# Performance work log

Hardware: AMD Instinct MI355X
Metric: run time of the kernel (lower is better)

## Reference

```python
import jax, jax.numpy as jnp
import numpy as np

EPS = 1e-6
SIGMA_C = 2.0
PAD = 0
VOCAB = 100
D_EMB = 384


def setup_inputs() -> dict:
    key = jax.random.key(0)
    k1, k2, k3 = jax.random.split(key, 3)
    B, L = 32, 1025  # L odd so durs[:,1::2] and durs[:,2::2] align
    text = jax.random.randint(k1, (B, L), 0, VOCAB)
    durs = jax.random.randint(k2, (B, L), 0, 4)
    emb_table = jax.random.normal(k3, (VOCAB, D_EMB), dtype=jnp.float32)
    return {"text": text, "durs": durs, "emb_table": emb_table, "total_time": 2048}


def reference(text, durs, emb_table, total_time):
    # --- merge blank/token pairs (as in GaussianEmbedding.forward) ---
    text_m = jnp.concatenate([text[:, :1], text[:, 1::2]], axis=1)              # [B,N]
    durs_m = jnp.concatenate([durs[:, :1], durs[:, 1::2] + durs[:, 2::2]], axis=1)  # [B,N]
    embed = emb_table[text_m]                                                    # [B,N,E]

    # --- Gaussian length regulation ---
    d = durs_m.astype(jnp.float32)
    cum = jnp.cumsum(d, axis=-1)                 # [B,N] end times
    c = cum - 0.5 * d                            # [B,N] token centers
    sig = d / SIGMA_C + EPS                      # [B,N]
    t = jnp.arange(total_time, dtype=jnp.float32) + 0.5  # [T] frame midpoints

    # Normal pdf weights [B,T,N]
    z = (t[None, :, None] - c[:, None, :]) / sig[:, None, :]
    w = jnp.exp(-0.5 * z * z) / (sig[:, None, :] * jnp.sqrt(2.0 * jnp.pi))
    # zero weight for pad tokens, normalize over tokens
    w = jnp.where((text_m == PAD)[:, None, :], 0.0, w)
    w = w / (w.sum(-1, keepdims=True) + EPS)
    # zero frames beyond each sample's total duration
    valid = t[None, :] < cum[:, -1:]             # [B,T]
    w = jnp.where(valid[..., None], w, 0.0)

    return jnp.einsum('btn,bne->bte', w, embed)  # [B,T,E]
```

## Files before the change

### kernel.cpp

```cpp
#include <hip/hip_runtime.h>
#include <hip/hip_bf16.h>

#define BATCH 32
#define LSEQ 1025
#define TT 2048
#define NTOK 513
#define EMB 384
#define FT 32
#define WMAX 64
#define INV_SQRT_2PI 0.3989422804014327f

__device__ inline float* scan513(float* src, float* dst) {
  for (int off = 1; off < NTOK; off <<= 1) {
    for (int i = threadIdx.x; i < NTOK; i += 256) {
      float v = src[i];
      if (i >= off) v += src[i - off];
      dst[i] = v;
    }
    __syncthreads();
    float* t = src; src = dst; dst = t;
  }
  return src;
}

__global__ __launch_bounds__(256) void prep_kernel(
    const int* __restrict__ text, const int* __restrict__ durs,
    float2* __restrict__ kept, int* __restrict__ counts,
    float* __restrict__ totals) {
  const int b = blockIdx.x;
  const int tid = threadIdx.x;
  __shared__ float s_a[NTOK], s_b[NTOK];
  __shared__ float s_c[NTOK];
  __shared__ float s_d[NTOK];
  __shared__ int s_tok[NTOK];

  const int* tb = text + b * LSEQ;
  const int* db = durs + b * LSEQ;
  for (int n = tid; n < NTOK; n += 256) {
    int dm, tk;
    if (n == 0) { dm = db[0]; tk = tb[0]; }
    else { dm = db[2 * n - 1] + db[2 * n]; tk = tb[2 * n - 1]; }
    s_d[n] = (float)dm;
    s_a[n] = (float)dm;
    s_tok[n] = tk;
  }
  __syncthreads();
  float* cum = scan513(s_a, s_b);
  for (int n = tid; n < NTOK; n += 256) {
    s_c[n] = cum[n] - 0.5f * s_d[n];
  }
  if (tid == 0) totals[b] = cum[NTOK - 1];
  __syncthreads();
  float* flagbuf = (cum == s_a) ? s_a : s_b;
  float* other = (cum == s_a) ? s_b : s_a;
  for (int n = tid; n < NTOK; n += 256) {
    flagbuf[n] = (s_d[n] >= 1.0f && s_tok[n] != 0) ? 1.0f : 0.0f;
  }
  __syncthreads();
  float* incl = scan513(flagbuf, other);
  for (int n = tid; n < NTOK; n += 256) {
    float d = s_d[n];
    int tk = s_tok[n];
    if (d >= 1.0f && tk != 0) {
      int pos = (int)incl[n] - 1;
      int packed = ((int)d << 17) | (tk * EMB);
      kept[b * NTOK + pos] = make_float2(s_c[n], __int_as_float(packed));
    }
  }
  if (tid == 0) counts[b] = (int)incl[NTOK - 1];
}

__global__ __launch_bounds__(384) void frames_kernel(
    const float2* __restrict__ kept, const int* __restrict__ counts,
    const float* __restrict__ totals, const float* __restrict__ emb,
    float* __restrict__ out) {
  const int t0 = blockIdx.x * FT;
  const int b = blockIdx.y;
  const int tid = threadIdx.x;
  const int g = tid / 96;
  const int q = tid % 96;
  const int fbase = g * 8;

  __shared__ float4 s_tk[WMAX];
  __shared__ float s_w[WMAX][FT];
  __shared__ float s_sum[FT];
  __shared__ int s_cnt;

  const int M = counts[b];
  const float total = totals[b];
  const float2* kb = kept + b * NTOK;

  const float tileLo = (float)t0 + 0.5f;
  const float tileHi = (float)t0 + 31.5f;
  const bool tile_valid = tileLo < total;

  int lo = 0, hi = 0;
  if (tile_valid) {
    const float loB = (float)t0 - 40.5f;
    const float hiB = (float)t0 + 72.5f;
    int l = 0, r = M;
    while (l < r) { int m = (l + r) >> 1; if (kb[m].x < loB) l = m + 1; else r = m; }
    lo = l;
    r = M;
    while (l < r) { int m = (l + r) >> 1; if (kb[m].x <= hiB) l = m + 1; else r = m; }
    hi = l;
  }

  if (tid < FT) s_sum[tid] = 0.f;

  float4 acc[8];
#pragma unroll
  for (int k = 0; k < 8; ++k) acc[k] = make_float4(0.f, 0.f, 0.f, 0.f);

  const float t0f = (float)t0 + 0.5f;

  for (int pos = lo; pos < hi; pos += WMAX) {
    const int cand = min(hi - pos, WMAX);
    __syncthreads();
    if (tid < 64) {
      bool touch = false;
      float cc = 0.f, df = 0.f;
      int packed = 0;
      if (tid < cand) {
        float2 kv = kb[pos + tid];
        cc = kv.x;
        packed = __float_as_int(kv.y);
        df = (float)(packed >> 17);
        const float reach = 6.7f * df + 1e-4f;
        touch = (cc + reach >= tileLo) && (cc - reach <= tileHi);
      }
      const unsigned long long mask = __ballot(touch);
      if (touch) {
        const int slot = __popcll(mask & ((1ull << (tid & 63)) - 1));
        const float inv_sig = 1.0f / (0.5f * df + 1e-6f);
        s_tk[slot] = make_float4(cc, inv_sig, INV_SQRT_2PI * inv_sig,
                                 __int_as_float(packed & 0x1FFFF));
      }
      if (tid == 0) s_cnt = __popcll(mask);
    }
    __syncthreads();
    const int cnt = s_cnt;

    const int pairs = cnt * FT;
    for (int idx = tid; idx < pairs; idx += 384) {
      const int n = idx >> 5, f = idx & (FT - 1);
      const float4 tk = s_tk[n];
      const float z = (t0f + (float)f - tk.x) * tk.y;
      s_w[n][f] = tk.z * __expf(-0.5f * z * z);
    }
    __syncthreads();

    if (tid < FT) {
      float s = 0.f;
      for (int n = 0; n < cnt; ++n) s += s_w[n][tid];
      s_sum[tid] += s;
    }

    for (int n = 0; n < cnt; ++n) {
      const float4 tk = s_tk[n];
      const float4 v = *(const float4*)(emb + __float_as_int(tk.w) + q * 4);
      const float4 w0 = *(const float4*)&s_w[n][fbase];
      const float4 w1 = *(const float4*)&s_w[n][fbase + 4];
      acc[0].x += w0.x * v.x; acc[0].y += w0.x * v.y;
      acc[0].z += w0.x * v.z; acc[0].w += w0.x * v.w;
      acc[1].x += w0.y * v.x; acc[1].y += w0.y * v.y;
      acc[1].z += w0.y * v.z; acc[1].w += w0.y * v.w;
      acc[2].x += w0.z * v.x; acc[2].y += w0.z * v.y;
      acc[2].z += w0.z * v.z; acc[2].w += w0.z * v.w;
      acc[3].x += w0.w * v.x; acc[3].y += w0.w * v.y;
      acc[3].z += w0.w * v.z; acc[3].w += w0.w * v.w;
      acc[4].x += w1.x * v.x; acc[4].y += w1.x * v.y;
      acc[4].z += w1.x * v.z; acc[4].w += w1.x * v.w;
      acc[5].x += w1.y * v.x; acc[5].y += w1.y * v.y;
      acc[5].z += w1.y * v.z; acc[5].w += w1.y * v.w;
      acc[6].x += w1.z * v.x; acc[6].y += w1.z * v.y;
      acc[6].z += w1.z * v.z; acc[6].w += w1.z * v.w;
      acc[7].x += w1.w * v.x; acc[7].y += w1.w * v.y;
      acc[7].z += w1.w * v.z; acc[7].w += w1.w * v.w;
    }
  }
  __syncthreads();

  float* obase = out + ((size_t)b * TT + t0 + fbase) * EMB + q * 4;
#pragma unroll
  for (int k = 0; k < 8; ++k) {
    const float tf = t0f + (float)(fbase + k);
    const float fac = (tf < total) ? 1.0f / (s_sum[fbase + k] + 1e-6f) : 0.0f;
    *(float4*)(obase + (size_t)k * EMB) =
        make_float4(acc[k].x * fac, acc[k].y * fac,
                    acc[k].z * fac, acc[k].w * fac);
  }
}

extern "C" void kernel_launch(void* const* d_in, const int* in_sizes, int n_in,
                              void* d_out, int out_size, void* d_ws,
                              size_t ws_size, hipStream_t stream) {
  const int* text = (const int*)d_in[0];
  const int* durs = (const int*)d_in[1];
  const float* emb = (const float*)d_in[2];
  float* out = (float*)d_out;

  float2* kept = (float2*)d_ws;
  int* counts = (int*)(kept + BATCH * NTOK);
  float* totals = (float*)(counts + BATCH);

  prep_kernel<<<BATCH, 256, 0, stream>>>(text, durs, kept, counts, totals);
  frames_kernel<<<dim3(TT / FT, BATCH), 384, 0, stream>>>(kept, counts, totals,
                                                          emb, out);
}
```

Measured before the change: 139.1 us.

## Halve frame tile, load token window once, fold weight sums into registers

Frame tiles shrink from 32 to 16 frames per block, with 192 threads per block and twice as many blocks. The per-chunk ballot/compaction loop is replaced by a single load of the whole candidate token window, capped at 104 entries. The per-frame normalisation sum is now accumulated in registers by each thread rather than in a shared-memory reduction. This removes several barriers and the serial sum pass, but any window wider than 104 tokens is silently truncated, and tokens outside the reach test now cost extra exp and FMA work.

```diff
diff --git a/kernel.cpp b/kernel.cpp
--- a/kernel.cpp
+++ b/kernel.cpp
@@ -6,8 +6,8 @@
 #define TT 2048
 #define NTOK 513
 #define EMB 384
-#define FT 32
-#define WMAX 64
+#define FT 16
+#define WMAX 104
 #define INV_SQRT_2PI 0.3989422804014327f
 
 __device__ inline float* scan513(float* src, float* dst) {
@@ -70,7 +70,7 @@
   if (tid == 0) counts[b] = (int)incl[NTOK - 1];
 }
 
-__global__ __launch_bounds__(384) void frames_kernel(
+__global__ __launch_bounds__(192) void frames_kernel(
     const float2* __restrict__ kept, const int* __restrict__ counts,
     const float* __restrict__ totals, const float* __restrict__ emb,
     float* __restrict__ out) {
@@ -83,109 +83,83 @@
 
   __shared__ float4 s_tk[WMAX];
   __shared__ float s_w[WMAX][FT];
-  __shared__ float s_sum[FT];
-  __shared__ int s_cnt;
 
   const int M = counts[b];
   const float total = totals[b];
   const float2* kb = kept + b * NTOK;
+  const float t0f = (float)t0 + 0.5f;
 
-  const float tileLo = (float)t0 + 0.5f;
-  const float tileHi = (float)t0 + 31.5f;
-  const bool tile_valid = tileLo < total;
-
-  int lo = 0, hi = 0;
-  if (tile_valid) {
+  int lo = 0, win = 0;
+  if (t0f < total) {
     const float loB = (float)t0 - 40.5f;
-    const float hiB = (float)t0 + 72.5f;
+    const float hiB = (float)t0 + 56.5f;
     int l = 0, r = M;
     while (l < r) { int m = (l + r) >> 1; if (kb[m].x < loB) l = m + 1; else r = m; }
     lo = l;
     r = M;
     while (l < r) { int m = (l + r) >> 1; if (kb[m].x <= hiB) l = m + 1; else r = m; }
-    hi = l;
+    win = l - lo;
+    if (win > WMAX) win = WMAX;
   }
 
-  if (tid < FT) s_sum[tid] = 0.f;
+  if (tid < win) {
+    float2 kv = kb[lo + tid];
+    int packed = __float_as_int(kv.y);
+    float df = (float)(packed >> 17);
+    float inv_sig = 1.0f / (0.5f * df + 1e-6f);
+    s_tk[tid] = make_float4(kv.x, inv_sig, INV_SQRT_2PI * inv_sig,
+                            __int_as_float(packed & 0x1FFFF));
+  }
+  __syncthreads();
+
+  const int pairs = win * FT;
+  for (int idx = tid; idx < pairs; idx += 192) {
+    const int n = idx >> 4, f = idx & (FT - 1);
+    const float4 tk = s_tk[n];
+    const float z = (t0f + (float)f - tk.x) * tk.y;
+    s_w[n][f] = tk.z * __expf(-0.5f * z * z);
+  }
+  __syncthreads();
 
   float4 acc[8];
+  float wsum[8];
 #pragma unroll
-  for (int k = 0; k < 8; ++k) acc[k] = make_float4(0.f, 0.f, 0.f, 0.f);
+  for (int k = 0; k < 8; ++k) {
+    acc[k] = make_float4(0.f, 0.f, 0.f, 0.f);
+    wsum[k] = 0.f;
+  }
 
-  const float t0f = (float)t0 + 0.5f;
-
-  for (int pos = lo; pos < hi; pos += WMAX) {
-    const int cand = min(hi - pos, WMAX);
-    __syncthreads();
-    if (tid < 64) {
-      bool touch = false;
-      float cc = 0.f, df = 0.f;
-      int packed = 0;
-      if (tid < cand) {
-        float2 kv = kb[pos + tid];
-        cc = kv.x;
-        packed = __float_as_int(kv.y);
-        df = (float)(packed >> 17);
-        const float reach = 6.7f * df + 1e-4f;
-        touch = (cc + reach >= tileLo) && (cc - reach <= tileHi);
-      }
-      const unsigned long long mask = __ballot(touch);
-      if (touch) {
-        const int slot = __popcll(mask & ((1ull << (tid & 63)) - 1));
-        const float inv_sig = 1.0f / (0.5f * df + 1e-6f);
-        s_tk[slot] = make_float4(cc, inv_sig, INV_SQRT_2PI * inv_sig,
-                                 __int_as_float(packed & 0x1FFFF));
-      }
-      if (tid == 0) s_cnt = __popcll(mask);
-    }
-    __syncthreads();
-    const int cnt = s_cnt;
-
-    const int pairs = cnt * FT;
-    for (int idx = tid; idx < pairs; idx += 384) {
-      const int n = idx >> 5, f = idx & (FT - 1);
-      const float4 tk = s_tk[n];
-      const float z = (t0f + (float)f - tk.x) * tk.y;
-      s_w[n][f] = tk.z * __expf(-0.5f * z * z);
-    }
-    __syncthreads();
-
-    if (tid < FT) {
-      float s = 0.f;
-      for (int n = 0; n < cnt; ++n) s += s_w[n][tid];
-      s_sum[tid] += s;
-    }
-
-    for (int n = 0; n < cnt; ++n) {
-      const float4 tk = s_tk[n];
-      const float4 v = *(const float4*)(emb + __float_as_int(tk.w) + q * 4);
-      const float4 w0 = *(const float4*)&s_w[n][fbase];
-      const float4 w1 = *(const float4*)&s_w[n][fbase + 4];
-      acc[0].x += w0.x * v.x; acc[0].y += w0.x * v.y;
-      acc[0].z += w0.x * v.z; acc[0].w += w0.x * v.w;
-      acc[1].x += w0.y * v.x; acc[1].y += w0.y * v.y;
-      acc[1].z += w0.y * v.z; acc[1].w += w0.y * v.w;
-      acc[2].x += w0.z * v.x; acc[2].y += w0.z * v.y;
-      acc[2].z += w0.z * v.z; acc[2].w += w0.z * v.w;
-      acc[3].x += w0.w * v.x; acc[3].y += w0.w * v.y;
-      acc[3].z += w0.w * v.z; acc[3].w += w0.w * v.w;
-      acc[4].x += w1.x * v.x; acc[4].y += w1.x * v.y;
-      acc[4].z += w1.x * v.z; acc[4].w += w1.x * v.w;
-      acc[5].x += w1.y * v.x; acc[5].y += w1.y * v.y;
-      acc[5].z += w1.y * v.z; acc[5].w += w1.y * v.w;
-      acc[6].x += w1.z * v.x; acc[6].y += w1.z * v.y;
-      acc[6].z += w1.z * v.z; acc[6].w += w1.z * v.w;
-      acc[7].x += w1.w * v.x; acc[7].y += w1.w * v.y;
-      acc[7].z += w1.w * v.z; acc[7].w += w1.w * v.w;
-    }
+#pragma unroll 2
+  for (int n = 0; n < win; ++n) {
+    const float4 tk = s_tk[n];
+    const float4 v = *(const float4*)(emb + __float_as_int(tk.w) + q * 4);
+    const float4 w0 = *(const float4*)&s_w[n][fbase];
+    const float4 w1 = *(const float4*)&s_w[n][fbase + 4];
+    wsum[0] += w0.x; wsum[1] += w0.y; wsum[2] += w0.z; wsum[3] += w0.w;
+    wsum[4] += w1.x; wsum[5] += w1.y; wsum[6] += w1.z; wsum[7] += w1.w;
+    acc[0].x += w0.x * v.x; acc[0].y += w0.x * v.y;
+    acc[0].z += w0.x * v.z; acc[0].w += w0.x * v.w;
+    acc[1].x += w0.y * v.x; acc[1].y += w0.y * v.y;
+    acc[1].z += w0.y * v.z; acc[1].w += w0.y * v.w;
+    acc[2].x += w0.z * v.x; acc[2].y += w0.z * v.y;
+    acc[2].z += w0.z * v.z; acc[2].w += w0.z * v.w;
+    acc[3].x += w0.w * v.x; acc[3].y += w0.w * v.y;
+    acc[3].z += w0.w * v.z; acc[3].w += w0.w * v.w;
+    acc[4].x += w1.x * v.x; acc[4].y += w1.x * v.y;
+    acc[4].z += w1.x * v.z; acc[4].w += w1.x * v.w;
+    acc[5].x += w1.y * v.x; acc[5].y += w1.y * v.y;
+    acc[5].z += w1.y * v.z; acc[5].w += w1.y * v.w;
+    acc[6].x += w1.z * v.x; acc[6].y += w1.z * v.y;
+    acc[6].z += w1.z * v.z; acc[6].w += w1.z * v.w;
+    acc[7].x += w1.w * v.x; acc[7].y += w1.w * v.y;
+    acc[7].z += w1.w * v.z; acc[7].w += w1.w * v.w;
   }
-  __syncthreads();
 
   float* obase = out + ((size_t)b * TT + t0 + fbase) * EMB + q * 4;
 #pragma unroll
   for (int k = 0; k < 8; ++k) {
     const float tf = t0f + (float)(fbase + k);
-    const float fac = (tf < total) ? 1.0f / (s_sum[fbase + k] + 1e-6f) : 0.0f;
+    const float fac = (tf < total) ? 1.0f / (wsum[k] + 1e-6f) : 0.0f;
     *(float4*)(obase + (size_t)k * EMB) =
         make_float4(acc[k].x * fac, acc[k].y * fac,
                     acc[k].z * fac, acc[k].w * fac);
@@ -205,6 +179,6 @@
   float* totals = (float*)(counts + BATCH);
 
   prep_kernel<<<BATCH, 256, 0, stream>>>(text, durs, kept, counts, totals);
-  frames_kernel<<<dim3(TT / FT, BATCH), 384, 0, stream>>>(kept, counts, totals,
+  frames_kernel<<<dim3(TT / FT, BATCH), 192, 0, stream>>>(kept, counts, totals,
                                                           emb, out);
 }
```

After: 133.7 us. -3.9%, faster.
